# Performance work log

Hardware: AMD Instinct MI355X
Metric: run time of the kernel (lower is better)

The kernel has to match this reference:

```python
import jax, jax.numpy as jnp
import numpy as np

B, N, C_X, D_MODEL, D_OUT, S = 32, 4096, 1, 64, 1, 2
D_IN = C_X + D_MODEL  # 65, channels entering graph_conv


def setup_inputs() -> dict:
    key = jax.random.key(0)
    ks = jax.random.split(key, 8)
    x = jax.random.normal(ks[0], (B, C_X, N), dtype=jnp.float32)
    h = jax.random.normal(ks[1], (B, D_MODEL, N), dtype=jnp.float32)
    # stacked support matrices (fwd/bwd normalized adjacency), used as a list of supports
    adj = jax.random.uniform(ks[2], (S, N, N), dtype=jnp.float32) / N
    # graph_conv.mlp : Conv2d(S*D_IN -> D_MODEL, 1x1)
    W_mlp = jax.random.normal(ks[3], (D_MODEL, S * D_IN), dtype=jnp.float32) / np.sqrt(S * D_IN)
    b_mlp = jnp.zeros((D_MODEL,), jnp.float32)
    # lin_out : Conv1d(2*D_MODEL -> D_MODEL, k=1)
    W_lin = jax.random.normal(ks[4], (D_MODEL, 2 * D_MODEL), dtype=jnp.float32) / np.sqrt(2 * D_MODEL)
    b_lin = jnp.zeros((D_MODEL,), jnp.float32)
    # read_out : Conv1d(2*D_MODEL -> D_OUT, k=1)
    W_read = jax.random.normal(ks[5], (D_OUT, 2 * D_MODEL), dtype=jnp.float32) / np.sqrt(2 * D_MODEL)
    b_read = jnp.zeros((D_OUT,), jnp.float32)
    prelu_a = jnp.array(0.25, jnp.float32)  # nn.PReLU() default: single shared slope
    return {"x": x, "h": h, "adj": adj, "W_mlp": W_mlp, "b_mlp": b_mlp,
            "W_lin": W_lin, "b_lin": b_lin, "W_read": W_read, "b_read": b_read,
            "prelu_a": prelu_a}


def conv1x1(W, b, x):
    # x: [B, C_in, N] -> [B, C_out, N]
    return jnp.einsum('oc,bcn->bon', W, x) + b[None, :, None]


def reference(x, h, adj, W_mlp, b_mlp, W_lin, b_lin, W_read, b_read, prelu_a):
    # x: [B, C_X, N], h: [B, D_MODEL, N], adj: [S, N, N]
    x_in = jnp.concatenate([x, h], axis=1)  # [B, D_IN, N]
    # SpatialConvOrderK (order=1, include_self=False):
    # out[b,c,w] per support s = sum_v x_in[b,c,v] * adj[s,w,v]
    hops = jnp.einsum('bcv,swv->bscw', x_in, adj)  # [B, S, D_IN, N]
    feats = hops.reshape(B, S * D_IN, N)           # channel-cat over supports
    out = conv1x1(W_mlp, b_mlp, feats)             # [B, D_MODEL, N]
    out = jnp.concatenate([out, h], axis=1)        # [B, 2*D_MODEL, N]
    out = conv1x1(W_lin, b_lin, out)               # [B, D_MODEL, N]
    out = jnp.where(out >= 0, out, prelu_a * out)  # PReLU
    out = jnp.concatenate([out, h], axis=1)        # [B, 2*D_MODEL, N]
    return (conv1x1(W_read, b_read, out), out)
```

## Files before the change

### kernel.cpp

```cpp
#include <hip/hip_runtime.h>
#include <cstdint>

#define N_NODES 4096
#define DM 64
#define K_DIM 8192
#define M_DIM 2048

typedef unsigned short bf16u;
using bf16x8  = __attribute__((ext_vector_type(8))) short;
using floatx4 = __attribute__((ext_vector_type(4))) float;

__device__ inline bf16u f2bf(float f) {
  uint32_t u = __float_as_uint(f);
  u += 0x7FFF + ((u >> 16) & 1);
  return (bf16u)(u >> 16);
}

#define GLOAD_LDS16(gp, lp)                                                     \
  __builtin_amdgcn_global_load_lds(                                             \
      reinterpret_cast<const __attribute__((address_space(1))) void*>(          \
          reinterpret_cast<uintptr_t>(gp)),                                     \
      reinterpret_cast<__attribute__((address_space(3))) void*>(                \
          (uint32_t)reinterpret_cast<uintptr_t>(lp)),                           \
      16, 0, 0)

__global__ __launch_bounds__(256) void k_adj2bt(const float* __restrict__ adj,
                                                bf16u* __restrict__ BT) {
  uint32_t idx = blockIdx.x * 256u + threadIdx.x;
  uint32_t v8 = idx & 511u;
  uint32_t w  = (idx >> 9) & 4095u;
  uint32_t s  = idx >> 21;
  const float4* src = reinterpret_cast<const float4*>(adj) + (size_t)idx * 2;
  float4 f0 = src[0], f1 = src[1];
  union { bf16u h[8]; uint4 u4; } pk;
  pk.h[0] = f2bf(f0.x); pk.h[1] = f2bf(f0.y); pk.h[2] = f2bf(f0.z); pk.h[3] = f2bf(f0.w);
  pk.h[4] = f2bf(f1.x); pk.h[5] = f2bf(f1.y); pk.h[6] = f2bf(f1.z); pk.h[7] = f2bf(f1.w);
  *reinterpret_cast<uint4*>(BT + ((size_t)w * K_DIM + s * N_NODES + v8 * 8)) = pk.u4;
}

__global__ __launch_bounds__(256) void k_mkA(const float* __restrict__ x,
                                             const float* __restrict__ h,
                                             const float* __restrict__ Wmlp,
                                             bf16u* __restrict__ A) {
  __shared__ __align__(16) float Ws[DM * 68];
  uint32_t bi = blockIdx.x;
  uint32_t v0 = (bi & 15u) * 256u;
  uint32_t s  = (bi >> 4) & 1u;
  uint32_t b  = bi >> 5;
  for (uint32_t t = threadIdx.x; t < DM * 68; t += 256) {
    uint32_t d = t / 68u, c = t % 68u;
    Ws[t] = (c < 65u) ? Wmlp[d * 130u + s * 65u + c] : 0.f;
  }
  __syncthreads();

  const uint32_t tv = threadIdx.x & 63u;
  const uint32_t td = threadIdx.x >> 6;
  const uint32_t v  = v0 + tv * 4u;

  float acc[16][4];
#pragma unroll
  for (int d = 0; d < 16; ++d)
#pragma unroll
    for (int k = 0; k < 4; ++k) acc[d][k] = 0.f;

  for (int c0 = 0; c0 < 64; c0 += 4) {
    float4 in4[4];
#pragma unroll
    for (int j = 0; j < 4; ++j) {
      int c = c0 + j;
      const float* src = (c == 0) ? (x + (size_t)b * N_NODES + v)
                                  : (h + ((size_t)b * DM + (c - 1)) * N_NODES + v);
      in4[j] = *reinterpret_cast<const float4*>(src);
    }
#pragma unroll
    for (int d = 0; d < 16; ++d) {
      const float4 w4 = *reinterpret_cast<const float4*>(&Ws[(td * 16 + d) * 68 + c0]);
      acc[d][0] += w4.x * in4[0].x + w4.y * in4[1].x + w4.z * in4[2].x + w4.w * in4[3].x;
      acc[d][1] += w4.x * in4[0].y + w4.y * in4[1].y + w4.z * in4[2].y + w4.w * in4[3].y;
      acc[d][2] += w4.x * in4[0].z + w4.y * in4[1].z + w4.z * in4[2].z + w4.w * in4[3].z;
      acc[d][3] += w4.x * in4[0].w + w4.y * in4[1].w + w4.z * in4[2].w + w4.w * in4[3].w;
    }
  }
  {
    float4 in4 = *reinterpret_cast<const float4*>(h + ((size_t)b * DM + 63) * N_NODES + v);
#pragma unroll
    for (int d = 0; d < 16; ++d) {
      float w = Ws[(td * 16 + d) * 68 + 64];
      acc[d][0] += w * in4.x; acc[d][1] += w * in4.y;
      acc[d][2] += w * in4.z; acc[d][3] += w * in4.w;
    }
  }
#pragma unroll
  for (int d = 0; d < 16; ++d) {
    union { bf16u h4[4]; uint2 u2; } pk;
#pragma unroll
    for (int k = 0; k < 4; ++k) pk.h4[k] = f2bf(acc[d][k]);
    *reinterpret_cast<uint2*>(A + (size_t)(b * DM + td * 16 + d) * K_DIM + s * N_NODES + v) = pk.u2;
  }
}

__global__ void k_gemm(const bf16u* __restrict__ A, const bf16u* __restrict__ BT,
                       float* __restrict__ C) {
  __shared__ __align__(16) bf16u As[128 * 32];
  __shared__ __align__(16) bf16u Bs[128 * 32];
  const int tid  = threadIdx.x;
  const int lane = tid & 63;
  const int wave = tid >> 6;
  const int wr = wave >> 1, wc = wave & 1;
  const int m0 = blockIdx.y * 128, n0 = blockIdx.x * 128;
  const int row_s = tid >> 2;
  const int col_s = (tid & 3) * 8;

  const bf16u* Ag0 = A  + (size_t)(m0 + row_s)      * K_DIM + col_s;
  const bf16u* Ag1 = A  + (size_t)(m0 + 64 + row_s) * K_DIM + col_s;
  const bf16u* Bg0 = BT + (size_t)(n0 + row_s)      * K_DIM + col_s;
  const bf16u* Bg1 = BT + (size_t)(n0 + 64 + row_s) * K_DIM + col_s;

  bf16u* AsW0 = As + wave * 512;
  bf16u* AsW1 = As + 2048 + wave * 512;
  bf16u* BsW0 = Bs + wave * 512;
  bf16u* BsW1 = Bs + 2048 + wave * 512;

  floatx4 acc[4][4];
#pragma unroll
  for (int i = 0; i < 4; ++i)
#pragma unroll
    for (int j = 0; j < 4; ++j) acc[i][j] = (floatx4){0.f, 0.f, 0.f, 0.f};

  const int fRow = lane & 15;
  const int fQ   = lane >> 4;

  for (int k0 = 0; k0 < K_DIM; k0 += 32) {
    GLOAD_LDS16(Ag0 + k0, AsW0);
    GLOAD_LDS16(Ag1 + k0, AsW1);
    GLOAD_LDS16(Bg0 + k0, BsW0);
    GLOAD_LDS16(Bg1 + k0, BsW1);
    __syncthreads();

    bf16x8 af[4], bfr[4];
#pragma unroll
    for (int i = 0; i < 4; ++i)
      af[i] = *reinterpret_cast<const bf16x8*>(&As[(wr * 64 + i * 16 + fRow) * 32 + fQ * 8]);
#pragma unroll
    for (int j = 0; j < 4; ++j)
      bfr[j] = *reinterpret_cast<const bf16x8*>(&Bs[(wc * 64 + j * 16 + fRow) * 32 + fQ * 8]);
#pragma unroll
    for (int i = 0; i < 4; ++i)
#pragma unroll
      for (int j = 0; j < 4; ++j)
        acc[i][j] = __builtin_amdgcn_mfma_f32_16x16x32_bf16(af[i], bfr[j], acc[i][j], 0, 0, 0);
    __syncthreads();
  }

  const int cr = (lane >> 4) * 4;
  const int cc = lane & 15;
#pragma unroll
  for (int i = 0; i < 4; ++i)
#pragma unroll
    for (int j = 0; j < 4; ++j) {
      float* Cp = C + (size_t)(m0 + wr * 64 + i * 16 + cr) * N_NODES
                    + (n0 + wc * 64 + j * 16 + cc);
#pragma unroll
      for (int r = 0; r < 4; ++r) Cp[(size_t)r * N_NODES] = acc[i][j][r];
    }
}

__global__ __launch_bounds__(256) void k_epilogue(
    const float* __restrict__ Cpre, const float* __restrict__ h,
    const float* __restrict__ bmlp, const float* __restrict__ Wlin,
    const float* __restrict__ blin, const float* __restrict__ Wread,
    const float* __restrict__ bread, const float* __restrict__ pa,
    float* __restrict__ out0, float* __restrict__ out1) {
  __shared__ __align__(16) float sW[DM * 132];
  __shared__ float sbm[DM], sbl[DM], sWr[128];
  __shared__ float psum[3 * 256];
  for (uint32_t t = threadIdx.x; t < DM * 128; t += 256) {
    uint32_t d = t >> 7, c = t & 127u;
    sW[d * 132 + c] = Wlin[t];
  }
  if (threadIdx.x < DM) { sbm[threadIdx.x] = bmlp[threadIdx.x]; sbl[threadIdx.x] = blin[threadIdx.x]; }
  if (threadIdx.x < 128) sWr[threadIdx.x] = Wread[threadIdx.x];
  __syncthreads();

  uint32_t bi = blockIdx.x;
  uint32_t n0 = (bi & 15u) * 256u;
  uint32_t b  = bi >> 4;
  const uint32_t tv = threadIdx.x & 63u;
  const uint32_t td = threadIdx.x >> 6;
  const uint32_t n  = n0 + tv * 4u;

  float acc[16][4];
#pragma unroll
  for (int d = 0; d < 16; ++d) {
    float bl = sbl[td * 16 + d];
#pragma unroll
    for (int k = 0; k < 4; ++k) acc[d][k] = bl;
  }

  for (int c0 = 0; c0 < 64; c0 += 4) {
    float4 in4[4];
#pragma unroll
    for (int j = 0; j < 4; ++j) {
      float4 v = *reinterpret_cast<const float4*>(Cpre + ((size_t)b * DM + (c0 + j)) * N_NODES + n);
      float bm = sbm[c0 + j];
      v.x += bm; v.y += bm; v.z += bm; v.w += bm;
      in4[j] = v;
    }
#pragma unroll
    for (int d = 0; d < 16; ++d) {
      const float4 w4 = *reinterpret_cast<const float4*>(&sW[(td * 16 + d) * 132 + c0]);
      acc[d][0] += w4.x * in4[0].x + w4.y * in4[1].x + w4.z * in4[2].x + w4.w * in4[3].x;
      acc[d][1] += w4.x * in4[0].y + w4.y * in4[1].y + w4.z * in4[2].y + w4.w * in4[3].y;
      acc[d][2] += w4.x * in4[0].z + w4.y * in4[1].z + w4.z * in4[2].z + w4.w * in4[3].z;
      acc[d][3] += w4.x * in4[0].w + w4.y * in4[1].w + w4.z * in4[2].w + w4.w * in4[3].w;
    }
  }
  for (int c0 = 0; c0 < 64; c0 += 4) {
    float4 in4[4];
#pragma unroll
    for (int j = 0; j < 4; ++j)
      in4[j] = *reinterpret_cast<const float4*>(h + ((size_t)b * DM + (c0 + j)) * N_NODES + n);
#pragma unroll
    for (int d = 0; d < 16; ++d) {
      const float4 w4 = *reinterpret_cast<const float4*>(&sW[(td * 16 + d) * 132 + 64 + c0]);
      acc[d][0] += w4.x * in4[0].x + w4.y * in4[1].x + w4.z * in4[2].x + w4.w * in4[3].x;
      acc[d][1] += w4.x * in4[0].y + w4.y * in4[1].y + w4.z * in4[2].y + w4.w * in4[3].y;
      acc[d][2] += w4.x * in4[0].z + w4.y * in4[1].z + w4.z * in4[2].z + w4.w * in4[3].z;
      acc[d][3] += w4.x * in4[0].w + w4.y * in4[1].w + w4.z * in4[2].w + w4.w * in4[3].w;
    }
  }

  const float a = pa[0];
  float r[4] = {0.f, 0.f, 0.f, 0.f};
  float* o1b = out1 + (size_t)b * 128 * N_NODES + n;
#pragma unroll
  for (int d = 0; d < 16; ++d) {
    float4 o2;
    o2.x = acc[d][0] >= 0.f ? acc[d][0] : a * acc[d][0];
    o2.y = acc[d][1] >= 0.f ? acc[d][1] : a * acc[d][1];
    o2.z = acc[d][2] >= 0.f ? acc[d][2] : a * acc[d][2];
    o2.w = acc[d][3] >= 0.f ? acc[d][3] : a * acc[d][3];
    *reinterpret_cast<float4*>(o1b + (size_t)(td * 16 + d) * N_NODES) = o2;
    float wr = sWr[td * 16 + d];
    r[0] += wr * o2.x; r[1] += wr * o2.y; r[2] += wr * o2.z; r[3] += wr * o2.w;
  }
#pragma unroll
  for (int d = 0; d < 16; ++d) {
    float4 hv = *reinterpret_cast<const float4*>(h + ((size_t)b * DM + td * 16 + d) * N_NODES + n);
    *reinterpret_cast<float4*>(o1b + (size_t)(64 + td * 16 + d) * N_NODES) = hv;
    float wr = sWr[64 + td * 16 + d];
    r[0] += wr * hv.x; r[1] += wr * hv.y; r[2] += wr * hv.z; r[3] += wr * hv.w;
  }
  if (td > 0) {
#pragma unroll
    for (int k = 0; k < 4; ++k) psum[(td - 1) * 256 + tv * 4 + k] = r[k];
  }
  __syncthreads();
  if (td == 0) {
    float br = bread[0];
#pragma unroll
    for (int k = 0; k < 4; ++k)
      r[k] += br + psum[tv * 4 + k] + psum[256 + tv * 4 + k] + psum[512 + tv * 4 + k];
    float4 o0; o0.x = r[0]; o0.y = r[1]; o0.z = r[2]; o0.w = r[3];
    *reinterpret_cast<float4*>(out0 + (size_t)b * N_NODES + n) = o0;
  }
}

extern "C" void kernel_launch(void* const* d_in, const int* in_sizes, int n_in,
                              void* d_out, int out_size, void* d_ws, size_t ws_size,
                              hipStream_t stream) {
  const float* x     = (const float*)d_in[0];
  const float* h     = (const float*)d_in[1];
  const float* adj   = (const float*)d_in[2];
  const float* Wmlp  = (const float*)d_in[3];
  const float* bmlp  = (const float*)d_in[4];
  const float* Wlin  = (const float*)d_in[5];
  const float* blin  = (const float*)d_in[6];
  const float* Wread = (const float*)d_in[7];
  const float* bread = (const float*)d_in[8];
  const float* pa    = (const float*)d_in[9];

  char* ws = (char*)d_ws;
  bf16u* Abuf  = (bf16u*)ws;
  bf16u* BTbuf = (bf16u*)(ws + 33554432ull);
  float* Cbuf  = (float*)(ws + 100663296ull);
  float* out0 = (float*)d_out;
  float* out1 = out0 + 131072;

  hipLaunchKernelGGL(k_adj2bt,   dim3(16384),  dim3(256), 0, stream, adj, BTbuf);
  hipLaunchKernelGGL(k_mkA,      dim3(1024),   dim3(256), 0, stream, x, h, Wmlp, Abuf);
  hipLaunchKernelGGL(k_gemm,     dim3(32, 16), dim3(256), 0, stream, Abuf, BTbuf, Cbuf);
  hipLaunchKernelGGL(k_epilogue, dim3(512),    dim3(256), 0, stream, Cbuf, h, bmlp,
                     Wlin, blin, Wread, bread, pa, out0, out1);
}
```

Measured before the change: 500.6 us.

## Switch adjacency GEMM to FP8 MFMA with split-K and fused prep kernel

Adjacency and the projected activations are now quantized to FP8 (adjacency pre-scaled by 4096) instead of bf16, and the GEMM uses the scaled 16x16x128 f8f6f4 MFMA with a 128-wide K step. This halves operand bytes and doubles the math rate per instruction. K is split across two z-slices whose partial results go to separate buffers, and the epilogue sums and rescales them. The two prep kernels are merged into one launch. FP8 precision may add accuracy error, and the split-K adds an extra output buffer read in the epilogue.

```diff
diff --git a/kernel.cpp b/kernel.cpp
--- a/kernel.cpp
+++ b/kernel.cpp
@@ -6,15 +6,9 @@
 #define K_DIM 8192
 #define M_DIM 2048
 
-typedef unsigned short bf16u;
-using bf16x8  = __attribute__((ext_vector_type(8))) short;
+typedef uint8_t u8;
+using i32x8   = __attribute__((ext_vector_type(8))) int;
 using floatx4 = __attribute__((ext_vector_type(4))) float;
-
-__device__ inline bf16u f2bf(float f) {
-  uint32_t u = __float_as_uint(f);
-  u += 0x7FFF + ((u >> 16) & 1);
-  return (bf16u)(u >> 16);
-}
 
 #define GLOAD_LDS16(gp, lp)                                                     \
   __builtin_amdgcn_global_load_lds(                                             \
@@ -24,29 +18,37 @@
           (uint32_t)reinterpret_cast<uintptr_t>(lp)),                           \
       16, 0, 0)
 
-__global__ __launch_bounds__(256) void k_adj2bt(const float* __restrict__ adj,
-                                                bf16u* __restrict__ BT) {
-  uint32_t idx = blockIdx.x * 256u + threadIdx.x;
-  uint32_t v8 = idx & 511u;
-  uint32_t w  = (idx >> 9) & 4095u;
-  uint32_t s  = idx >> 21;
-  const float4* src = reinterpret_cast<const float4*>(adj) + (size_t)idx * 2;
-  float4 f0 = src[0], f1 = src[1];
-  union { bf16u h[8]; uint4 u4; } pk;
-  pk.h[0] = f2bf(f0.x); pk.h[1] = f2bf(f0.y); pk.h[2] = f2bf(f0.z); pk.h[3] = f2bf(f0.w);
-  pk.h[4] = f2bf(f1.x); pk.h[5] = f2bf(f1.y); pk.h[6] = f2bf(f1.z); pk.h[7] = f2bf(f1.w);
-  *reinterpret_cast<uint4*>(BT + ((size_t)w * K_DIM + s * N_NODES + v8 * 8)) = pk.u4;
-}
-
-__global__ __launch_bounds__(256) void k_mkA(const float* __restrict__ x,
-                                             const float* __restrict__ h,
-                                             const float* __restrict__ Wmlp,
-                                             bf16u* __restrict__ A) {
+__device__ inline int pk_fp8x4(float f0, float f1, float f2, float f3) {
+  int r = __builtin_amdgcn_cvt_pk_fp8_f32(f0, f1, 0, false);
+  r     = __builtin_amdgcn_cvt_pk_fp8_f32(f2, f3, r, true);
+  return r;
+}
+
+__global__ __launch_bounds__(256) void k_prep(const float* __restrict__ adj,
+                                              u8* __restrict__ BT8,
+                                              const float* __restrict__ x,
+                                              const float* __restrict__ h,
+                                              const float* __restrict__ Wmlp,
+                                              u8* __restrict__ A8) {
   __shared__ __align__(16) float Ws[DM * 68];
   uint32_t bi = blockIdx.x;
-  uint32_t v0 = (bi & 15u) * 256u;
-  uint32_t s  = (bi >> 4) & 1u;
-  uint32_t b  = bi >> 5;
+  if (bi < 16384u) {
+    uint32_t idx = bi * 256u + threadIdx.x;
+    uint32_t v8 = idx & 511u;
+    uint32_t w  = (idx >> 9) & 4095u;
+    uint32_t s  = idx >> 21;
+    const float4* src = reinterpret_cast<const float4*>(adj) + (size_t)idx * 2;
+    float4 f0 = src[0], f1 = src[1];
+    uint2 pk;
+    pk.x = (uint32_t)pk_fp8x4(f0.x * 4096.f, f0.y * 4096.f, f0.z * 4096.f, f0.w * 4096.f);
+    pk.y = (uint32_t)pk_fp8x4(f1.x * 4096.f, f1.y * 4096.f, f1.z * 4096.f, f1.w * 4096.f);
+    *reinterpret_cast<uint2*>(BT8 + ((size_t)w * K_DIM + s * N_NODES + v8 * 8)) = pk;
+    return;
+  }
+  uint32_t b2 = bi - 16384u;
+  uint32_t v0 = (b2 & 15u) * 256u;
+  uint32_t s  = (b2 >> 4) & 1u;
+  uint32_t b  = b2 >> 5;
   for (uint32_t t = threadIdx.x; t < DM * 68; t += 256) {
     uint32_t d = t / 68u, c = t % 68u;
     Ws[t] = (c < 65u) ? Wmlp[d * 130u + s * 65u + c] : 0.f;
@@ -92,34 +94,29 @@
   }
 #pragma unroll
   for (int d = 0; d < 16; ++d) {
-    union { bf16u h4[4]; uint2 u2; } pk;
-#pragma unroll
-    for (int k = 0; k < 4; ++k) pk.h4[k] = f2bf(acc[d][k]);
-    *reinterpret_cast<uint2*>(A + (size_t)(b * DM + td * 16 + d) * K_DIM + s * N_NODES + v) = pk.u2;
-  }
-}
-
-__global__ void k_gemm(const bf16u* __restrict__ A, const bf16u* __restrict__ BT,
+    int p = pk_fp8x4(acc[d][0], acc[d][1], acc[d][2], acc[d][3]);
+    *reinterpret_cast<int*>(A8 + (size_t)(b * DM + td * 16 + d) * K_DIM + s * N_NODES + v) = p;
+  }
+}
+
+__global__ void k_gemm(const u8* __restrict__ A, const u8* __restrict__ BT,
                        float* __restrict__ C) {
-  __shared__ __align__(16) bf16u As[128 * 32];
-  __shared__ __align__(16) bf16u Bs[128 * 32];
+  __shared__ __align__(32) u8 As[4][128][32];
+  __shared__ __align__(32) u8 Bs[4][128][32];
   const int tid  = threadIdx.x;
   const int lane = tid & 63;
   const int wave = tid >> 6;
   const int wr = wave >> 1, wc = wave & 1;
   const int m0 = blockIdx.y * 128, n0 = blockIdx.x * 128;
-  const int row_s = tid >> 2;
-  const int col_s = (tid & 3) * 8;
-
-  const bf16u* Ag0 = A  + (size_t)(m0 + row_s)      * K_DIM + col_s;
-  const bf16u* Ag1 = A  + (size_t)(m0 + 64 + row_s) * K_DIM + col_s;
-  const bf16u* Bg0 = BT + (size_t)(n0 + row_s)      * K_DIM + col_s;
-  const bf16u* Bg1 = BT + (size_t)(n0 + 64 + row_s) * K_DIM + col_s;
-
-  bf16u* AsW0 = As + wave * 512;
-  bf16u* AsW1 = As + 2048 + wave * 512;
-  bf16u* BsW0 = Bs + wave * 512;
-  bf16u* BsW1 = Bs + 2048 + wave * 512;
+  const size_t kb = (size_t)blockIdx.z * 4096;
+
+  const int srow = lane >> 1;
+  const int shalf = (lane & 1) * 16;
+  const u8* Ag = A  + (size_t)(m0 + wave * 32 + srow) * K_DIM + kb + shalf;
+  const u8* Bg = BT + (size_t)(n0 + wave * 32 + srow) * K_DIM + kb + shalf;
+  u8* AsB[4]; u8* BsB[4];
+#pragma unroll
+  for (int q = 0; q < 4; ++q) { AsB[q] = &As[q][wave * 32][0]; BsB[q] = &Bs[q][wave * 32][0]; }
 
   floatx4 acc[4][4];
 #pragma unroll
@@ -127,46 +124,50 @@
 #pragma unroll
     for (int j = 0; j < 4; ++j) acc[i][j] = (floatx4){0.f, 0.f, 0.f, 0.f};
 
-  const int fRow = lane & 15;
-  const int fQ   = lane >> 4;
-
-  for (int k0 = 0; k0 < K_DIM; k0 += 32) {
-    GLOAD_LDS16(Ag0 + k0, AsW0);
-    GLOAD_LDS16(Ag1 + k0, AsW1);
-    GLOAD_LDS16(Bg0 + k0, BsW0);
-    GLOAD_LDS16(Bg1 + k0, BsW1);
+  const int fm = lane & 15;
+  const int fq = lane >> 4;
+  const int SC1 = 0x7F7F7F7F;
+
+  for (int k0 = 0; k0 < 4096; k0 += 128) {
+#pragma unroll
+    for (int q = 0; q < 4; ++q) GLOAD_LDS16(Ag + k0 + q * 32, AsB[q]);
+#pragma unroll
+    for (int q = 0; q < 4; ++q) GLOAD_LDS16(Bg + k0 + q * 32, BsB[q]);
     __syncthreads();
 
-    bf16x8 af[4], bfr[4];
+    i32x8 af[4], bfr[4];
 #pragma unroll
     for (int i = 0; i < 4; ++i)
-      af[i] = *reinterpret_cast<const bf16x8*>(&As[(wr * 64 + i * 16 + fRow) * 32 + fQ * 8]);
+      af[i] = *reinterpret_cast<const i32x8*>(&As[fq][wr * 64 + i * 16 + fm][0]);
 #pragma unroll
     for (int j = 0; j < 4; ++j)
-      bfr[j] = *reinterpret_cast<const bf16x8*>(&Bs[(wc * 64 + j * 16 + fRow) * 32 + fQ * 8]);
+      bfr[j] = *reinterpret_cast<const i32x8*>(&Bs[fq][wc * 64 + j * 16 + fm][0]);
 #pragma unroll
     for (int i = 0; i < 4; ++i)
 #pragma unroll
       for (int j = 0; j < 4; ++j)
-        acc[i][j] = __builtin_amdgcn_mfma_f32_16x16x32_bf16(af[i], bfr[j], acc[i][j], 0, 0, 0);
+        acc[i][j] = __builtin_amdgcn_mfma_scale_f32_16x16x128_f8f6f4(
+            af[i], bfr[j], acc[i][j], 0, 0, 0, SC1, 0, SC1);
     __syncthreads();
   }
 
+  float* Cz = C + (size_t)blockIdx.z * M_DIM * N_NODES;
   const int cr = (lane >> 4) * 4;
   const int cc = lane & 15;
 #pragma unroll
   for (int i = 0; i < 4; ++i)
 #pragma unroll
     for (int j = 0; j < 4; ++j) {
-      float* Cp = C + (size_t)(m0 + wr * 64 + i * 16 + cr) * N_NODES
-                    + (n0 + wc * 64 + j * 16 + cc);
+      float* Cp = Cz + (size_t)(m0 + wr * 64 + i * 16 + cr) * N_NODES
+                     + (n0 + wc * 64 + j * 16 + cc);
 #pragma unroll
       for (int r = 0; r < 4; ++r) Cp[(size_t)r * N_NODES] = acc[i][j][r];
     }
 }
 
 __global__ __launch_bounds__(256) void k_epilogue(
-    const float* __restrict__ Cpre, const float* __restrict__ h,
+    const float* __restrict__ C0, const float* __restrict__ C1,
+    const float* __restrict__ h,
     const float* __restrict__ bmlp, const float* __restrict__ Wlin,
     const float* __restrict__ blin, const float* __restrict__ Wread,
     const float* __restrict__ bread, const float* __restrict__ pa,
@@ -188,6 +189,7 @@
   const uint32_t tv = threadIdx.x & 63u;
   const uint32_t td = threadIdx.x >> 6;
   const uint32_t n  = n0 + tv * 4u;
+  const float KS = 1.0f / 4096.0f;
 
   float acc[16][4];
 #pragma unroll
@@ -201,9 +203,13 @@
     float4 in4[4];
 #pragma unroll
     for (int j = 0; j < 4; ++j) {
-      float4 v = *reinterpret_cast<const float4*>(Cpre + ((size_t)b * DM + (c0 + j)) * N_NODES + n);
+      size_t off = ((size_t)b * DM + (c0 + j)) * N_NODES + n;
+      float4 v0 = *reinterpret_cast<const float4*>(C0 + off);
+      float4 v1 = *reinterpret_cast<const float4*>(C1 + off);
       float bm = sbm[c0 + j];
-      v.x += bm; v.y += bm; v.z += bm; v.w += bm;
+      float4 v;
+      v.x = (v0.x + v1.x) * KS + bm; v.y = (v0.y + v1.y) * KS + bm;
+      v.z = (v0.z + v1.z) * KS + bm; v.w = (v0.w + v1.w) * KS + bm;
       in4[j] = v;
     }
 #pragma unroll
@@ -281,15 +287,16 @@
   const float* pa    = (const float*)d_in[9];
 
   char* ws = (char*)d_ws;
-  bf16u* Abuf  = (bf16u*)ws;
-  bf16u* BTbuf = (bf16u*)(ws + 33554432ull);
-  float* Cbuf  = (float*)(ws + 100663296ull);
+  u8*    Abuf  = (u8*)ws;
+  u8*    BTbuf = (u8*)(ws + (16ull << 20));
+  float* C0    = (float*)(ws + (48ull << 20));
+  float* C1    = (float*)(ws + (80ull << 20));
   float* out0 = (float*)d_out;
   float* out1 = out0 + 131072;
 
-  hipLaunchKernelGGL(k_adj2bt,   dim3(16384),  dim3(256), 0, stream, adj, BTbuf);
-  hipLaunchKernelGGL(k_mkA,      dim3(1024),   dim3(256), 0, stream, x, h, Wmlp, Abuf);
-  hipLaunchKernelGGL(k_gemm,     dim3(32, 16), dim3(256), 0, stream, Abuf, BTbuf, Cbuf);
-  hipLaunchKernelGGL(k_epilogue, dim3(512),    dim3(256), 0, stream, Cbuf, h, bmlp,
+  hipLaunchKernelGGL(k_prep,     dim3(17408),     dim3(256), 0, stream,
+                     adj, BTbuf, x, h, Wmlp, Abuf);
+  hipLaunchKernelGGL(k_gemm,     dim3(32, 16, 2), dim3(256), 0, stream, Abuf, BTbuf, C0);
+  hipLaunchKernelGGL(k_epilogue, dim3(512),       dim3(256), 0, stream, C0, C1, h, bmlp,
                      Wlin, blin, Wread, bread, pa, out0, out1);
 }
```

Result: faster. 422.9 us (-15.5%).
